# Kernel optimization log

Measured on AMD Instinct MI355X. Metric: run time of the kernel, lower is better.

The kernel has to match this reference:

```python
import jax, jax.numpy as jnp
import numpy as np

N_PAPER, N_AUTHOR, E = 100000, 50000, 1000000
D_PAPER, D_AUTHOR, HID, OUT = 256, 128, 256, 349


def setup_inputs() -> dict:
    key = jax.random.key(0)
    ks = jax.random.split(key, 16)
    s = 0.05
    return {
        'x_paper': jax.random.normal(ks[0], (N_PAPER, D_PAPER), jnp.float32),
        'x_author': jax.random.normal(ks[1], (N_AUTHOR, D_AUTHOR), jnp.float32),
        'cites': jax.random.randint(ks[2], (2, E), 0, N_PAPER, jnp.int64 if jax.config.jax_enable_x64 else jnp.int32),
        'writes_src': jax.random.randint(ks[3], (E,), 0, N_AUTHOR),
        'writes_dst': jax.random.randint(ks[4], (E,), 0, N_PAPER),
        'gcn_W1': jax.random.normal(ks[5], (D_PAPER, HID), jnp.float32) * s,
        'gcn_b1': jnp.zeros((HID,), jnp.float32),
        'sage_Wl1': jax.random.normal(ks[6], (D_AUTHOR, HID), jnp.float32) * s,
        'sage_bl1': jnp.zeros((HID,), jnp.float32),
        'sage_Wr1': jax.random.normal(ks[7], (D_PAPER, HID), jnp.float32) * s,
        'gcn_W2': jax.random.normal(ks[8], (HID, HID), jnp.float32) * s,
        'gcn_b2': jnp.zeros((HID,), jnp.float32),
        'sage_Wl2': jax.random.normal(ks[9], (D_AUTHOR, HID), jnp.float32) * s,
        'sage_bl2': jnp.zeros((HID,), jnp.float32),
        'sage_Wr2': jax.random.normal(ks[10], (HID, HID), jnp.float32) * s,
        'lin_W': jax.random.normal(ks[11], (HID, OUT), jnp.float32) * s,
        'lin_b': jnp.zeros((OUT,), jnp.float32),
    }


def _gcn_conv(x, W, b, src, dst, n):
    # GCNConv with add_self_loops=True, symmetric normalization
    loop = jnp.arange(n, dtype=src.dtype)
    si = jnp.concatenate([src, loop])
    di = jnp.concatenate([dst, loop])
    deg = jax.ops.segment_sum(jnp.ones_like(di, x.dtype), di, n)
    dinv = jnp.where(deg > 0, jax.lax.rsqrt(jnp.maximum(deg, 1.0)), 0.0)
    norm = dinv[si] * dinv[di]  # [E+n]
    h = x @ W                   # [n, hid]
    out = jax.ops.segment_sum(h[si] * norm[:, None], di, n)
    return out + b


def _sage_conv(x_src, x_dst, Wl, bl, Wr, src, dst, n_dst):
    # SAGEConv: mean-aggregate neighbors -> lin_l, plus root lin_r (no bias)
    agg = jax.ops.segment_sum(x_src[src], dst, n_dst)
    cnt = jax.ops.segment_sum(jnp.ones_like(dst, x_src.dtype), dst, n_dst)
    mean = agg / jnp.maximum(cnt, 1.0)[:, None]
    return mean @ Wl + bl + x_dst @ Wr


def reference(x_paper, x_author, cites, writes_src, writes_dst,
              gcn_W1, gcn_b1, sage_Wl1, sage_bl1, sage_Wr1,
              gcn_W2, gcn_b2, sage_Wl2, sage_bl2, sage_Wr2,
              lin_W, lin_b):
    n = x_paper.shape[0]
    c_src, c_dst = cites[0], cites[1]
    # layer 1: HeteroConv with aggr='sum' over the two edge-type outputs
    p = jax.nn.relu(
        _gcn_conv(x_paper, gcn_W1, gcn_b1, c_src, c_dst, n)
        + _sage_conv(x_author, x_paper, sage_Wl1, sage_bl1, sage_Wr1, writes_src, writes_dst, n))
    # layer 2 (author features are never updated by these edge types)
    p = jax.nn.relu(
        _gcn_conv(p, gcn_W2, gcn_b2, c_src, c_dst, n)
        + _sage_conv(x_author, p, sage_Wl2, sage_bl2, sage_Wr2, writes_src, writes_dst, n))
    return p @ lin_W + lin_b
```

## Files before the change

kernel.cpp:

```cpp
#include <hip/hip_runtime.h>


#define DP   256
#define DA   128
#define HIDN 256
#define DOUT 349
#define NBKT 782
#define CHUNK 4096

typedef unsigned short u16;
typedef unsigned int u32;
typedef __attribute__((ext_vector_type(8))) short bf16x8;
typedef __attribute__((ext_vector_type(4))) float f32x4;

__device__ __forceinline__ u16 bf16_rn(float x) {
  union { float f; unsigned u; } v; v.f = x;
  unsigned r = v.u + 0x7FFFu + ((v.u >> 16) & 1u);
  return (u16)(r >> 16);
}
__device__ __forceinline__ float bf16f(u16 h) {
  union { float f; unsigned u; } v; v.u = ((unsigned)h) << 16; return v.f;
}
__device__ __forceinline__ unsigned pack2(float a, float b) {
  return (unsigned)bf16_rn(a) | ((unsigned)bf16_rn(b) << 16);
}

__device__ __forceinline__ void gload16(const void* g, void* lds) {
  __builtin_amdgcn_global_load_lds(
      (const __attribute__((address_space(1))) unsigned int*)g,
      (__attribute__((address_space(3))) unsigned int*)lds, 16, 0, 0);
}

#define SCAN_TPB 256
#define SCAN_VPT 8
#define SCAN_TILE 2048

__global__ void scan_local(const int* __restrict__ in, int* __restrict__ out,
                           int* __restrict__ bsum, int n) {
  __shared__ int sdata[SCAN_TPB];
  int t = threadIdx.x;
  int base = blockIdx.x * SCAN_TILE + t * SCAN_VPT;
  int v[SCAN_VPT];
  int sum = 0;
#pragma unroll
  for (int j = 0; j < SCAN_VPT; ++j) {
    int idx = base + j;
    v[j] = (idx < n) ? in[idx] : 0;
    sum += v[j];
  }
  sdata[t] = sum;
  __syncthreads();
  for (int off = 1; off < SCAN_TPB; off <<= 1) {
    int x = (t >= off) ? sdata[t - off] : 0;
    __syncthreads();
    sdata[t] += x;
    __syncthreads();
  }
  int prefix = sdata[t] - sum;
  if (t == SCAN_TPB - 1) bsum[blockIdx.x] = sdata[t];
  int run = prefix;
#pragma unroll
  for (int j = 0; j < SCAN_VPT; ++j) {
    int idx = base + j;
    if (idx < n) out[idx] = run;
    run += v[j];
  }
}

__global__ void scan_spine(int* __restrict__ bsum, int nb) {
  __shared__ int sdata[256];
  int t = threadIdx.x;
  int v = (t < nb) ? bsum[t] : 0;
  sdata[t] = v;
  __syncthreads();
  for (int off = 1; off < 256; off <<= 1) {
    int x = (t >= off) ? sdata[t - off] : 0;
    __syncthreads();
    sdata[t] += x;
    __syncthreads();
  }
  if (t < nb) bsum[t] = sdata[t] - v;
}

__global__ void scan_add(int* __restrict__ out, const int* __restrict__ bsum, int n) {
  int add = bsum[blockIdx.x];
  int base = blockIdx.x * SCAN_TILE + threadIdx.x * SCAN_VPT;
#pragma unroll
  for (int j = 0; j < SCAN_VPT; ++j) {
    int idx = base + j;
    if (idx < n) out[idx] += add;
  }
}

__global__ __launch_bounds__(256) void sort_pass1(
    const int* __restrict__ c_src, const int* __restrict__ c_dst,
    const int* __restrict__ w_srcP, const int* __restrict__ w_dstP,
    uint2* __restrict__ tmp, int* __restrict__ gcount, int* __restrict__ lofs,
    int E, int nch) {
  const int cg = blockIdx.x, t = threadIdx.x;
  const int et = cg >= nch;
  const int c = cg - et * nch;
  const int* src = et ? w_srcP : c_src;
  const int* dst = et ? w_dstP : c_dst;
  __shared__ u32 cnt[NBKT];
  __shared__ u32 ofs[NBKT];
  __shared__ u32 sdata[256];
  __shared__ uint2 stage[CHUNK];

  for (int i = t; i < NBKT; i += 256) cnt[i] = 0;
  __syncthreads();
  const int base = c * CHUNK;
#pragma unroll
  for (int j = 0; j < 16; ++j) {
    int i = t + j * 256, idx = base + i;
    if (idx < E) {
      uint2 e; e.x = (u32)src[idx]; e.y = (u32)dst[idx];
      stage[i] = e;
      atomicAdd(&cnt[e.y >> 7], 1u);
    }
  }
  __syncthreads();
  for (int i = t; i < NBKT; i += 256)
    gcount[((size_t)et * NBKT + i) * nch + c] = (int)cnt[i];
  u32 ssum = 0;
  const int b0 = t * 4;
#pragma unroll
  for (int j = 0; j < 4; ++j) {
    int i = b0 + j;
    if (i < NBKT) ssum += cnt[i];
  }
  sdata[t] = ssum;
  __syncthreads();
  for (int o = 1; o < 256; o <<= 1) {
    u32 x = (t >= o) ? sdata[t - o] : 0;
    __syncthreads();
    sdata[t] += x;
    __syncthreads();
  }
  u32 run = sdata[t] - ssum;
#pragma unroll
  for (int j = 0; j < 4; ++j) {
    int i = b0 + j;
    if (i < NBKT) { ofs[i] = run; run += cnt[i]; }
  }
  __syncthreads();
  for (int i = t; i < NBKT; i += 256) {
    lofs[((size_t)et * nch + c) * NBKT + i] = (int)ofs[i];
    cnt[i] = ofs[i];
  }
  __syncthreads();
  uint2* tout = tmp + (size_t)et * nch * CHUNK + base;
#pragma unroll
  for (int j = 0; j < 16; ++j) {
    int i = t + j * 256, idx = base + i;
    if (idx < E) {
      uint2 e = stage[i];
      u32 p = atomicAdd(&cnt[e.y >> 7], 1u);
      tout[p] = e;
    }
  }
}

#define MAXB 2560
__global__ __launch_bounds__(256) void sort_pass2(
    const uint2* __restrict__ tmp, const int* __restrict__ prefix,
    const int* __restrict__ gcount, const int* __restrict__ lofs,
    int* __restrict__ cSorted, int* __restrict__ cDeg, int* __restrict__ cOff,
    int* __restrict__ wSorted, int* __restrict__ wDeg, int* __restrict__ wOff,
    float* __restrict__ dinv,
    int E, int nch, int n, int nbk) {
  const int bg = blockIdx.x, t = threadIdx.x;
  const int et = bg >= nbk;
  const int b = bg - et * nbk;
  int* outSorted = et ? wSorted : cSorted;
  int* deg = et ? wDeg : cDeg;
  int* offArr = et ? wOff : cOff;
  __shared__ u32 est[MAXB];
  __shared__ u32 outl[MAXB];
  __shared__ u32 cnt[128], ofs[128];
  __shared__ u32 sdata[256];

  const int node0 = b << 7;
  const size_t bgl = (size_t)et * NBKT + b;
  const int ebaseG = prefix[bgl * nch];
  const int eendG = (bg == 2 * nbk - 1) ? 2 * E : prefix[(bgl + 1) * nch];
  const int ebase = ebaseG - et * E;
  const int esize = (eendG - et * E) - ebase;

  const uint2* tsrc = tmp + (size_t)et * nch * CHUNK;
  for (int c = t; c < nch; c += 256) {
    int g = lofs[((size_t)et * nch + c) * NBKT + b];
    int len = gcount[bgl * nch + c];
    int dp = prefix[bgl * nch + c] - ebaseG;
    for (int k = 0; k < len; ++k) {
      uint2 e = tsrc[(size_t)c * CHUNK + g + k];
      est[dp + k] = (e.x << 7) | (e.y & 127u);
    }
  }
  if (t < 128) cnt[t] = 0;
  __syncthreads();
  for (int i = t; i < esize; i += 256) atomicAdd(&cnt[est[i] & 127u], 1u);
  __syncthreads();
  u32 v = (t < 128) ? cnt[t] : 0;
  sdata[t] = v;
  __syncthreads();
  for (int o = 1; o < 256; o <<= 1) {
    u32 x = (t >= o) ? sdata[t - o] : 0;
    __syncthreads();
    sdata[t] += x;
    __syncthreads();
  }
  if (t < 128) ofs[t] = sdata[t] - v;
  __syncthreads();
  const int nNodes = (n - node0) < 128 ? (n - node0) : 128;
  if (t < nNodes) {
    deg[node0 + t] = (int)cnt[t];
    offArr[node0 + t] = ebase + (int)ofs[t];
    if (et == 0) dinv[node0 + t] = rsqrtf((float)(cnt[t] + 1));
  }
  __syncthreads();
  if (t < 128) cnt[t] = ofs[t];
  __syncthreads();
  for (int i = t; i < esize; i += 256) {
    u32 e = est[i];
    u32 p = atomicAdd(&cnt[e & 127u], 1u);
    outl[p] = e >> 7;
  }
  __syncthreads();
  for (int i = t; i < esize; i += 256) outSorted[ebase + i] = (int)outl[i];
}

__global__ void conv_bf16(const float* __restrict__ x, u16* __restrict__ o, int n8) {
  int i = blockIdx.x * blockDim.x + threadIdx.x;
  if (i >= n8) return;
  const float4* x4 = (const float4*)x;
  float4 v0 = x4[(size_t)i * 2];
  float4 v1 = x4[(size_t)i * 2 + 1];
  uint4 O;
  O.x = pack2(v0.x, v0.y);
  O.y = pack2(v0.z, v0.w);
  O.z = pack2(v1.x, v1.y);
  O.w = pack2(v1.z, v1.w);
  ((uint4*)o)[i] = O;
}

__global__ void prep_weight(const float* __restrict__ W, int K, int N, int Npad,
                            u16* __restrict__ Bt) {
  int idx = blockIdx.x * blockDim.x + threadIdx.x;
  int tot = Npad * K;
  if (idx >= tot) return;
  int n = idx / K, k = idx - n * K;
  float v = (n < N) ? W[(size_t)k * N + n] : 0.f;
  Bt[idx] = bf16_rn(v);
}

__global__ void pad_bias(const float* __restrict__ a, const float* __restrict__ b,
                         float* __restrict__ o, int n, int npad) {
  int i = blockIdx.x * blockDim.x + threadIdx.x;
  if (i < npad) o[i] = (i < n) ? (a[i] + (b ? b[i] : 0.f)) : 0.f;
}

__global__ void gather_fused(
    const u16* __restrict__ xin, const float* __restrict__ dinv,
    const int* __restrict__ c_off, const int* __restrict__ c_cnt,
    const int* __restrict__ c_sorted, u16* __restrict__ xout,
    const u16* __restrict__ xa16, const int* __restrict__ w_off,
    const int* __restrict__ w_cnt, const int* __restrict__ w_sorted,
    u16* __restrict__ mean, int n, int nbw) {
  const int lane = threadIdx.x & 63;
  if (blockIdx.x < nbw) {
    int wave = ((blockIdx.x * blockDim.x) >> 6) + (threadIdx.x >> 6);
    if (wave >= n) return;
    int d = wave;
    int start = c_off[d], cnt = c_cnt[d];
    float a0 = 0.f, a1 = 0.f, a2 = 0.f, a3 = 0.f;
    const uint2* base = (const uint2*)xin;
    for (int j0 = 0; j0 < cnt; j0 += 64) {
      int nn = cnt - j0; nn = nn < 64 ? nn : 64;
      int sl = (j0 + lane < cnt) ? c_sorted[start + j0 + lane] : 0;
      int jj = 0;
      for (; jj + 4 <= nn; jj += 4) {
        int s0 = __shfl(sl, jj), s1 = __shfl(sl, jj + 1);
        int s2 = __shfl(sl, jj + 2), s3 = __shfl(sl, jj + 3);
        float d0 = dinv[s0], d1 = dinv[s1], d2 = dinv[s2], d3 = dinv[s3];
        uint2 v0 = base[(size_t)s0 * 64 + lane];
        uint2 v1 = base[(size_t)s1 * 64 + lane];
        uint2 v2 = base[(size_t)s2 * 64 + lane];
        uint2 v3 = base[(size_t)s3 * 64 + lane];
        a0 = fmaf(bf16f((u16)v0.x), d0, a0); a1 = fmaf(bf16f((u16)(v0.x >> 16)), d0, a1);
        a2 = fmaf(bf16f((u16)v0.y), d0, a2); a3 = fmaf(bf16f((u16)(v0.y >> 16)), d0, a3);
        a0 = fmaf(bf16f((u16)v1.x), d1, a0); a1 = fmaf(bf16f((u16)(v1.x >> 16)), d1, a1);
        a2 = fmaf(bf16f((u16)v1.y), d1, a2); a3 = fmaf(bf16f((u16)(v1.y >> 16)), d1, a3);
        a0 = fmaf(bf16f((u16)v2.x), d2, a0); a1 = fmaf(bf16f((u16)(v2.x >> 16)), d2, a1);
        a2 = fmaf(bf16f((u16)v2.y), d2, a2); a3 = fmaf(bf16f((u16)(v2.y >> 16)), d2, a3);
        a0 = fmaf(bf16f((u16)v3.x), d3, a0); a1 = fmaf(bf16f((u16)(v3.x >> 16)), d3, a1);
        a2 = fmaf(bf16f((u16)v3.y), d3, a2); a3 = fmaf(bf16f((u16)(v3.y >> 16)), d3, a3);
      }
      for (; jj < nn; ++jj) {
        int s = __shfl(sl, jj);
        float ds = dinv[s];
        uint2 v = base[(size_t)s * 64 + lane];
        a0 = fmaf(bf16f((u16)v.x), ds, a0); a1 = fmaf(bf16f((u16)(v.x >> 16)), ds, a1);
        a2 = fmaf(bf16f((u16)v.y), ds, a2); a3 = fmaf(bf16f((u16)(v.y >> 16)), ds, a3);
      }
    }
    float dd = dinv[d];
    {
      uint2 v = base[(size_t)d * 64 + lane];
      a0 = fmaf(bf16f((u16)v.x), dd, a0); a1 = fmaf(bf16f((u16)(v.x >> 16)), dd, a1);
      a2 = fmaf(bf16f((u16)v.y), dd, a2); a3 = fmaf(bf16f((u16)(v.y >> 16)), dd, a3);
    }
    uint2 O;
    O.x = pack2(a0 * dd, a1 * dd);
    O.y = pack2(a2 * dd, a3 * dd);
    ((uint2*)xout)[(size_t)d * 64 + lane] = O;
  } else {
    int wave = (((blockIdx.x - nbw) * blockDim.x) >> 6) + (threadIdx.x >> 6);
    if (wave >= n) return;
    int d = wave;
    int start = w_off[d];
    int cnt = w_cnt[d];
    float ax = 0.f, ay = 0.f;
    const unsigned* xa = (const unsigned*)xa16;
    for (int j0 = 0; j0 < cnt; j0 += 64) {
      int nn = cnt - j0; nn = nn < 64 ? nn : 64;
      int sl = (j0 + lane < cnt) ? w_sorted[start + j0 + lane] : 0;
      int jj = 0;
      for (; jj + 4 <= nn; jj += 4) {
        int s0 = __shfl(sl, jj), s1 = __shfl(sl, jj + 1);
        int s2 = __shfl(sl, jj + 2), s3 = __shfl(sl, jj + 3);
        unsigned v0 = xa[(size_t)s0 * 64 + lane];
        unsigned v1 = xa[(size_t)s1 * 64 + lane];
        unsigned v2 = xa[(size_t)s2 * 64 + lane];
        unsigned v3 = xa[(size_t)s3 * 64 + lane];
        ax += bf16f((u16)v0) + bf16f((u16)v1) + bf16f((u16)v2) + bf16f((u16)v3);
        ay += bf16f((u16)(v0 >> 16)) + bf16f((u16)(v1 >> 16)) +
              bf16f((u16)(v2 >> 16)) + bf16f((u16)(v3 >> 16));
      }
      for (; jj < nn; ++jj) {
        int s = __shfl(sl, jj);
        unsigned v = xa[(size_t)s * 64 + lane];
        ax += bf16f((u16)v);
        ay += bf16f((u16)(v >> 16));
      }
    }
    float inv = 1.0f / (float)((cnt > 0) ? cnt : 1);
    ((unsigned*)mean)[(size_t)d * 64 + lane] = pack2(ax * inv, ay * inv);
  }
}

__global__ void agg_gcn(const u16* __restrict__ xin, const float* __restrict__ dinv,
                        const int* __restrict__ c_off, const int* __restrict__ c_cnt,
                        const int* __restrict__ c_sorted,
                        u16* __restrict__ xout, int n) {
  int wave = (blockIdx.x * blockDim.x + threadIdx.x) >> 6;
  int lane = threadIdx.x & 63;
  if (wave >= n) return;
  int d = wave;
  int start = c_off[d], cnt = c_cnt[d];
  float a0 = 0.f, a1 = 0.f, a2 = 0.f, a3 = 0.f;
  const uint2* base = (const uint2*)xin;
  for (int j0 = 0; j0 < cnt; j0 += 64) {
    int nn = cnt - j0; nn = nn < 64 ? nn : 64;
    int sl = (j0 + lane < cnt) ? c_sorted[start + j0 + lane] : 0;
    int jj = 0;
    for (; jj + 4 <= nn; jj += 4) {
      int s0 = __shfl(sl, jj), s1 = __shfl(sl, jj + 1);
      int s2 = __shfl(sl, jj + 2), s3 = __shfl(sl, jj + 3);
      float d0 = dinv[s0], d1 = dinv[s1], d2 = dinv[s2], d3 = dinv[s3];
      uint2 v0 = base[(size_t)s0 * 64 + lane];
      uint2 v1 = base[(size_t)s1 * 64 + lane];
      uint2 v2 = base[(size_t)s2 * 64 + lane];
      uint2 v3 = base[(size_t)s3 * 64 + lane];
      a0 = fmaf(bf16f((u16)v0.x), d0, a0); a1 = fmaf(bf16f((u16)(v0.x >> 16)), d0, a1);
      a2 = fmaf(bf16f((u16)v0.y), d0, a2); a3 = fmaf(bf16f((u16)(v0.y >> 16)), d0, a3);
      a0 = fmaf(bf16f((u16)v1.x), d1, a0); a1 = fmaf(bf16f((u16)(v1.x >> 16)), d1, a1);
      a2 = fmaf(bf16f((u16)v1.y), d1, a2); a3 = fmaf(bf16f((u16)(v1.y >> 16)), d1, a3);
      a0 = fmaf(bf16f((u16)v2.x), d2, a0); a1 = fmaf(bf16f((u16)(v2.x >> 16)), d2, a1);
      a2 = fmaf(bf16f((u16)v2.y), d2, a2); a3 = fmaf(bf16f((u16)(v2.y >> 16)), d2, a3);
      a0 = fmaf(bf16f((u16)v3.x), d3, a0); a1 = fmaf(bf16f((u16)(v3.x >> 16)), d3, a1);
      a2 = fmaf(bf16f((u16)v3.y), d3, a2); a3 = fmaf(bf16f((u16)(v3.y >> 16)), d3, a3);
    }
    for (; jj < nn; ++jj) {
      int s = __shfl(sl, jj);
      float ds = dinv[s];
      uint2 v = base[(size_t)s * 64 + lane];
      a0 = fmaf(bf16f((u16)v.x), ds, a0); a1 = fmaf(bf16f((u16)(v.x >> 16)), ds, a1);
      a2 = fmaf(bf16f((u16)v.y), ds, a2); a3 = fmaf(bf16f((u16)(v.y >> 16)), ds, a3);
    }
  }
  float dd = dinv[d];
  {
    uint2 v = base[(size_t)d * 64 + lane];
    a0 = fmaf(bf16f((u16)v.x), dd, a0); a1 = fmaf(bf16f((u16)(v.x >> 16)), dd, a1);
    a2 = fmaf(bf16f((u16)v.y), dd, a2); a3 = fmaf(bf16f((u16)(v.y >> 16)), dd, a3);
  }
  uint2 O;
  O.x = pack2(a0 * dd, a1 * dd);
  O.y = pack2(a2 * dd, a3 * dd);
  ((uint2*)xout)[(size_t)d * 64 + lane] = O;
}

template <int NSEG, bool F32OUT, int NC>
__global__ __launch_bounds__(256, 4) void gemm_bf16(
    const u16* __restrict__ A0, const u16* __restrict__ A1, const u16* __restrict__ A2,
    const u16* __restrict__ B0, const u16* __restrict__ B1, const u16* __restrict__ B2,
    const float* __restrict__ bias,
    u16* __restrict__ Cp, float* __restrict__ Cf,
    int M, int N) {
  __shared__ u16 Ah[2][4096];
  __shared__ u16 Bh[2][4096];

  const int t = threadIdx.x;
  const int wid = t >> 6, lane = t & 63;
  const int wr = wid >> 1, wc = wid & 1;
  const int lrow = lane & 15, kslot = lane >> 4;
  const int jsw = kslot ^ ((lrow >> 1) & 3);

  const int nb = gridDim.x;
  const int q = nb >> 3, r = nb & 7;
  const int xcd = blockIdx.x & 7, pos = blockIdx.x >> 3;
  const int lin = (xcd < r ? xcd * (q + 1) : r * (q + 1) + (xcd - r) * q) + pos;
  const int bx = lin / NC, by = lin - bx * NC;
  const int gm = bx * 128;
  const int gn = by * 128;

  const int s_r = lane >> 2;
  const int s_j = (lane & 3) ^ ((s_r >> 1) & 3);

  f32x4 acc[4][4];
  const f32x4 z4 = {0.f, 0.f, 0.f, 0.f};
#pragma unroll
  for (int m = 0; m < 4; ++m)
#pragma unroll
    for (int n = 0; n < 4; ++n) acc[m][n] = z4;

  const int NT = (NSEG == 3) ? 20 : 8;

  auto STAGE = [&](int tt, int half) {
    const u16* A;
    const u16* B;
    int rs, k0;
    if (NSEG == 3 && tt >= 16)     { A = A2; B = B2; rs = 128; k0 = (tt - 16) * 32; }
    else if (NSEG == 3 && tt >= 8) { A = A1; B = B1; rs = 256; k0 = (tt - 8) * 32; }
    else                           { A = A0; B = B0; rs = 256; k0 = tt * 32; }
    const int c = wid * 2;
#pragma unroll
    for (int cc = 0; cc < 2; ++cc) {
      int grow = gm + (c + cc) * 16 + s_r;
      grow = grow < M ? grow : M - 1;
      gload16(A + (size_t)grow * rs + (k0 + s_j * 8), &Ah[half][(c + cc) * 512]);
      int col = gn + (c + cc) * 16 + s_r;
      gload16(B + (size_t)col * rs + (k0 + s_j * 8), &Bh[half][(c + cc) * 512]);
    }
  };

  STAGE(0, 0);
  __syncthreads();

  for (int tt = 0; tt < NT; ++tt) {
    const int half = tt & 1;
    if (tt + 1 < NT) STAGE(tt + 1, half ^ 1);

    bf16x8 ah[4];
    const int ab = (wr * 64 + lrow) * 32 + jsw * 8;
#pragma unroll
    for (int m = 0; m < 4; ++m) ah[m] = *(const bf16x8*)&Ah[half][ab + m * 512];
    const int bb = (wc * 64 + lrow) * 32 + jsw * 8;
#pragma unroll
    for (int n = 0; n < 4; ++n) {
      bf16x8 bn = *(const bf16x8*)&Bh[half][bb + n * 512];
#pragma unroll
      for (int m = 0; m < 4; ++m)
        acc[m][n] = __builtin_amdgcn_mfma_f32_16x16x32_bf16(ah[m], bn, acc[m][n], 0, 0, 0);
    }
    __syncthreads();
  }

  const int col0 = gn + wc * 64 + lrow;
  const int row00 = gm + wr * 64 + kslot * 4;
#pragma unroll
  for (int m = 0; m < 4; ++m) {
#pragma unroll
    for (int i = 0; i < 4; ++i) {
      int row = row00 + m * 16 + i;
      if (row >= M) continue;
#pragma unroll
      for (int n = 0; n < 4; ++n) {
        int col = col0 + n * 16;
        float v = acc[m][n][i] + bias[col];
        if (F32OUT) {
          if (col < N) Cf[(size_t)row * N + col] = v;
        } else {
          Cp[(size_t)row * 256 + col] = bf16_rn(fmaxf(v, 0.f));
        }
      }
    }
  }
}

static inline size_t align_up(size_t x) { return (x + 255) & ~(size_t)255; }

extern "C" void kernel_launch(void* const* d_in, const int* in_sizes, int n_in,
                              void* d_out, int out_size, void* d_ws, size_t ws_size,
                              hipStream_t stream) {
  const float* x_paper  = (const float*)d_in[0];
  const float* x_author = (const float*)d_in[1];
  const int*   cites    = (const int*)d_in[2];
  const int*   w_src    = (const int*)d_in[3];
  const int*   w_dst    = (const int*)d_in[4];
  const float* W1  = (const float*)d_in[5];
  const float* b1  = (const float*)d_in[6];
  const float* Wl1 = (const float*)d_in[7];
  const float* bl1 = (const float*)d_in[8];
  const float* Wr1 = (const float*)d_in[9];
  const float* W2  = (const float*)d_in[10];
  const float* b2  = (const float*)d_in[11];
  const float* Wl2 = (const float*)d_in[12];
  const float* bl2 = (const float*)d_in[13];
  const float* Wr2 = (const float*)d_in[14];
  const float* linW = (const float*)d_in[15];
  const float* linb = (const float*)d_in[16];
  float* out = (float*)d_out;

  const int N = in_sizes[0] / DP;
  const int NA = in_sizes[1] / DA;
  const int E = in_sizes[3];
  const int* c_src = cites;
  const int* c_dst = cites + E;

  const int NCH = (E + CHUNK - 1) / CHUNK;
  const int NB = (N + 127) >> 7;
  const int GC2 = 2 * NB * NCH;

  char* w = (char*)d_ws;
  size_t off = 0;
  auto alloc = [&](size_t bytes) -> void* {
    void* p = w + off;
    off = align_up(off + bytes);
    return p;
  };
  int* deg_c      = (int*)alloc((size_t)N * 4);
  int* cnt_w      = (int*)alloc((size_t)N * 4);
  int* cites_off  = (int*)alloc((size_t)N * 4);
  int* writes_off = (int*)alloc((size_t)N * 4);
  int* c_sorted   = (int*)alloc((size_t)E * 4);
  int* w_sorted   = (int*)alloc((size_t)E * 4);
  uint2* tmpE     = (uint2*)alloc((size_t)2 * NCH * CHUNK * 8);
  int* gcount     = (int*)alloc((size_t)GC2 * 4);
  int* gprefix    = (int*)alloc((size_t)GC2 * 4);
  int* lofs       = (int*)alloc((size_t)2 * NCH * NBKT * 4);
  int* bsumA      = (int*)alloc(256 * 4);
  float* dinv     = (float*)alloc((size_t)N * 4);
  u16* xa16       = (u16*)alloc((size_t)NA * DA * 2);
  u16* meanA      = (u16*)alloc((size_t)N * DA * 2);
  u16* xp         = (u16*)alloc((size_t)N * 256 * 2);
  u16* xs         = (u16*)alloc((size_t)N * 256 * 2);
  u16* pb         = (u16*)alloc((size_t)N * 256 * 2);
  const int bsW = 256 * 256, bsL = 256 * 128, bsLin = 384 * 256;
  u16* BtW1  = (u16*)alloc((size_t)bsW * 2);
  u16* BtWr1 = (u16*)alloc((size_t)bsW * 2);
  u16* BtW2  = (u16*)alloc((size_t)bsW * 2);
  u16* BtWr2 = (u16*)alloc((size_t)bsW * 2);
  u16* BtWl1 = (u16*)alloc((size_t)bsL * 2);
  u16* BtWl2 = (u16*)alloc((size_t)bsL * 2);
  u16* BtLin = (u16*)alloc((size_t)bsLin * 2);
  float* biasR1  = (float*)alloc(256 * 4);
  float* biasR2  = (float*)alloc(256 * 4);
  float* biasLin = (float*)alloc(384 * 4);
  (void)ws_size; (void)n_in; (void)out_size;

  const int nsb2 = (GC2 + SCAN_TILE - 1) / SCAN_TILE;

  sort_pass1<<<2 * NCH, 256, 0, stream>>>(c_src, c_dst, w_src, w_dst,
                                          tmpE, gcount, lofs, E, NCH);
  scan_local<<<nsb2, SCAN_TPB, 0, stream>>>(gcount, gprefix, bsumA, GC2);
  scan_spine<<<1, 256, 0, stream>>>(bsumA, nsb2);
  scan_add<<<nsb2, SCAN_TPB, 0, stream>>>(gprefix, bsumA, GC2);
  sort_pass2<<<2 * NB, 256, 0, stream>>>(tmpE, gprefix, gcount, lofs,
                                         c_sorted, deg_c, cites_off,
                                         w_sorted, cnt_w, writes_off,
                                         dinv, E, NCH, N, NB);

  conv_bf16<<<(N * 32 + 255) / 256, 256, 0, stream>>>(x_paper, xp, N * 32);
  conv_bf16<<<(NA * 16 + 255) / 256, 256, 0, stream>>>(x_author, xa16, NA * 16);

  prep_weight<<<(bsW + 255) / 256, 256, 0, stream>>>(W1, 256, 256, 256, BtW1);
  prep_weight<<<(bsW + 255) / 256, 256, 0, stream>>>(Wr1, 256, 256, 256, BtWr1);
  prep_weight<<<(bsW + 255) / 256, 256, 0, stream>>>(W2, 256, 256, 256, BtW2);
  prep_weight<<<(bsW + 255) / 256, 256, 0, stream>>>(Wr2, 256, 256, 256, BtWr2);
  prep_weight<<<(bsL + 255) / 256, 256, 0, stream>>>(Wl1, 128, 256, 256, BtWl1);
  prep_weight<<<(bsL + 255) / 256, 256, 0, stream>>>(Wl2, 128, 256, 256, BtWl2);
  prep_weight<<<(bsLin + 255) / 256, 256, 0, stream>>>(linW, 256, DOUT, 384, BtLin);
  pad_bias<<<1, 256, 0, stream>>>(b1, bl1, biasR1, 256, 256);
  pad_bias<<<1, 256, 0, stream>>>(b2, bl2, biasR2, 256, 256);
  pad_bias<<<2, 256, 0, stream>>>(linb, nullptr, biasLin, DOUT, 384);

  const int nbWave = (N * 64 + 255) / 256;
  const int GX = (N + 127) / 128;

  gather_fused<<<2 * nbWave, 256, 0, stream>>>(
      xp, dinv, cites_off, deg_c, c_sorted, xs,
      xa16, writes_off, cnt_w, w_sorted, meanA, N, nbWave);
  gemm_bf16<3, false, 2><<<GX * 2, 256, 0, stream>>>(
      xs, xp, meanA, BtW1, BtWr1, BtWl1, biasR1, pb, nullptr, N, HIDN);
  agg_gcn<<<nbWave, 256, 0, stream>>>(pb, dinv, cites_off, deg_c, c_sorted, xs, N);
  gemm_bf16<3, false, 2><<<GX * 2, 256, 0, stream>>>(
      xs, pb, meanA, BtW2, BtWr2, BtWl2, biasR2, xp, nullptr, N, HIDN);
  gemm_bf16<1, true, 3><<<GX * 3, 256, 0, stream>>>(
      xp, nullptr, nullptr, BtLin, nullptr, nullptr, biasLin, nullptr, out, N, DOUT);
}
```

Measured before the change: 493.2 us.

## Pack sort payload into 32 bits, merge prep launches, deepen gather unroll

The sort passes now carry one packed 32-bit payload (src<<7 | dst&127) per edge plus a 16-bit bucket index in shared memory, which halves the temp-buffer traffic between sort_pass1 and sort_pass2. The ten separate conversion, weight-prep and bias kernels are merged into a single prep_all launch to cut launch overhead. The GCN and mean gather loops are moved into shared helpers and unrolled by 8 instead of 4 for more memory-level parallelism, at the cost of higher register pressure. The packed payload assumes source indices fit in 25 bits.

```diff
diff --git a/kernel.cpp b/kernel.cpp
--- a/kernel.cpp
+++ b/kernel.cpp
@@ -95,7 +95,7 @@
 __global__ __launch_bounds__(256) void sort_pass1(
     const int* __restrict__ c_src, const int* __restrict__ c_dst,
     const int* __restrict__ w_srcP, const int* __restrict__ w_dstP,
-    uint2* __restrict__ tmp, int* __restrict__ gcount, int* __restrict__ lofs,
+    u32* __restrict__ tmp, int* __restrict__ gcount, int* __restrict__ lofs,
     int E, int nch) {
   const int cg = blockIdx.x, t = threadIdx.x;
   const int et = cg >= nch;
@@ -105,7 +105,8 @@
   __shared__ u32 cnt[NBKT];
   __shared__ u32 ofs[NBKT];
   __shared__ u32 sdata[256];
-  __shared__ uint2 stage[CHUNK];
+  __shared__ u32 pay[CHUNK];
+  __shared__ u16 bkt[CHUNK];
 
   for (int i = t; i < NBKT; i += 256) cnt[i] = 0;
   __syncthreads();
@@ -114,9 +115,10 @@
   for (int j = 0; j < 16; ++j) {
     int i = t + j * 256, idx = base + i;
     if (idx < E) {
-      uint2 e; e.x = (u32)src[idx]; e.y = (u32)dst[idx];
-      stage[i] = e;
-      atomicAdd(&cnt[e.y >> 7], 1u);
+      u32 s = (u32)src[idx], d = (u32)dst[idx];
+      pay[i] = (s << 7) | (d & 127u);
+      bkt[i] = (u16)(d >> 7);
+      atomicAdd(&cnt[d >> 7], 1u);
     }
   }
   __syncthreads();
@@ -149,21 +151,20 @@
     cnt[i] = ofs[i];
   }
   __syncthreads();
-  uint2* tout = tmp + (size_t)et * nch * CHUNK + base;
+  u32* tout = tmp + (size_t)et * nch * CHUNK + base;
 #pragma unroll
   for (int j = 0; j < 16; ++j) {
     int i = t + j * 256, idx = base + i;
     if (idx < E) {
-      uint2 e = stage[i];
-      u32 p = atomicAdd(&cnt[e.y >> 7], 1u);
-      tout[p] = e;
+      u32 p = atomicAdd(&cnt[bkt[i]], 1u);
+      tout[p] = pay[i];
     }
   }
 }
 
 #define MAXB 2560
 __global__ __launch_bounds__(256) void sort_pass2(
-    const uint2* __restrict__ tmp, const int* __restrict__ prefix,
+    const u32* __restrict__ tmp, const int* __restrict__ prefix,
     const int* __restrict__ gcount, const int* __restrict__ lofs,
     int* __restrict__ cSorted, int* __restrict__ cDeg, int* __restrict__ cOff,
     int* __restrict__ wSorted, int* __restrict__ wDeg, int* __restrict__ wOff,
@@ -187,15 +188,13 @@
   const int ebase = ebaseG - et * E;
   const int esize = (eendG - et * E) - ebase;
 
-  const uint2* tsrc = tmp + (size_t)et * nch * CHUNK;
+  const u32* tsrc = tmp + (size_t)et * nch * CHUNK;
   for (int c = t; c < nch; c += 256) {
     int g = lofs[((size_t)et * nch + c) * NBKT + b];
     int len = gcount[bgl * nch + c];
     int dp = prefix[bgl * nch + c] - ebaseG;
-    for (int k = 0; k < len; ++k) {
-      uint2 e = tsrc[(size_t)c * CHUNK + g + k];
-      est[dp + k] = (e.x << 7) | (e.y & 127u);
-    }
+    for (int k = 0; k < len; ++k)
+      est[dp + k] = tsrc[(size_t)c * CHUNK + g + k];
   }
   if (t < 128) cnt[t] = 0;
   __syncthreads();
@@ -230,34 +229,159 @@
   for (int i = t; i < esize; i += 256) outSorted[ebase + i] = (int)outl[i];
 }
 
-__global__ void conv_bf16(const float* __restrict__ x, u16* __restrict__ o, int n8) {
-  int i = blockIdx.x * blockDim.x + threadIdx.x;
-  if (i >= n8) return;
-  const float4* x4 = (const float4*)x;
-  float4 v0 = x4[(size_t)i * 2];
-  float4 v1 = x4[(size_t)i * 2 + 1];
-  uint4 O;
-  O.x = pack2(v0.x, v0.y);
-  O.y = pack2(v0.z, v0.w);
-  O.z = pack2(v1.x, v1.y);
-  O.w = pack2(v1.z, v1.w);
-  ((uint4*)o)[i] = O;
-}
-
-__global__ void prep_weight(const float* __restrict__ W, int K, int N, int Npad,
-                            u16* __restrict__ Bt) {
-  int idx = blockIdx.x * blockDim.x + threadIdx.x;
+__global__ void prep_all(
+    const float* __restrict__ x_paper, const float* __restrict__ x_author,
+    u16* __restrict__ xp, u16* __restrict__ xa16,
+    const float* __restrict__ W1, const float* __restrict__ Wr1,
+    const float* __restrict__ W2, const float* __restrict__ Wr2,
+    const float* __restrict__ Wl1, const float* __restrict__ Wl2,
+    const float* __restrict__ linW,
+    u16* __restrict__ BtW1, u16* __restrict__ BtWr1,
+    u16* __restrict__ BtW2, u16* __restrict__ BtWr2,
+    u16* __restrict__ BtWl1, u16* __restrict__ BtWl2, u16* __restrict__ BtLin,
+    const float* __restrict__ b1, const float* __restrict__ bl1,
+    const float* __restrict__ b2, const float* __restrict__ bl2,
+    const float* __restrict__ linb,
+    float* __restrict__ biasR1, float* __restrict__ biasR2,
+    float* __restrict__ biasLin,
+    int N, int NA) {
+  const int R1 = (N * 32 + 255) / 256;
+  const int R2 = R1 + (NA * 16 + 255) / 256;
+  const int WB = 256 * 256 / 256;
+  const int LB = 256 * 128 / 256;
+  const int FB = 384 * 256 / 256;
+  int bid = blockIdx.x, t = threadIdx.x;
+
+  if (bid < R1) {
+    int i = bid * 256 + t;
+    if (i < N * 32) {
+      const float4* x4 = (const float4*)x_paper;
+      float4 v0 = x4[(size_t)i * 2];
+      float4 v1 = x4[(size_t)i * 2 + 1];
+      uint4 O;
+      O.x = pack2(v0.x, v0.y); O.y = pack2(v0.z, v0.w);
+      O.z = pack2(v1.x, v1.y); O.w = pack2(v1.z, v1.w);
+      ((uint4*)xp)[i] = O;
+    }
+    return;
+  }
+  if (bid < R2) {
+    int i = (bid - R1) * 256 + t;
+    if (i < NA * 16) {
+      const float4* x4 = (const float4*)x_author;
+      float4 v0 = x4[(size_t)i * 2];
+      float4 v1 = x4[(size_t)i * 2 + 1];
+      uint4 O;
+      O.x = pack2(v0.x, v0.y); O.y = pack2(v0.z, v0.w);
+      O.z = pack2(v1.x, v1.y); O.w = pack2(v1.z, v1.w);
+      ((uint4*)xa16)[i] = O;
+    }
+    return;
+  }
+  int wb = bid - R2;
+  const float* W; u16* Bt; int K, Nn, Npad;
+  if      (wb < WB)                  { W = W1;  Bt = BtW1;  K = 256; Nn = 256; Npad = 256; }
+  else if ((wb -= WB) < WB)          { W = Wr1; Bt = BtWr1; K = 256; Nn = 256; Npad = 256; }
+  else if ((wb -= WB) < WB)          { W = W2;  Bt = BtW2;  K = 256; Nn = 256; Npad = 256; }
+  else if ((wb -= WB) < WB)          { W = Wr2; Bt = BtWr2; K = 256; Nn = 256; Npad = 256; }
+  else if ((wb -= WB) < LB)          { W = Wl1; Bt = BtWl1; K = 128; Nn = 256; Npad = 256; }
+  else if ((wb -= LB) < LB)          { W = Wl2; Bt = BtWl2; K = 128; Nn = 256; Npad = 256; }
+  else if ((wb -= LB) < FB)          { W = linW; Bt = BtLin; K = 256; Nn = DOUT; Npad = 384; }
+  else {
+    if (t < 256) {
+      biasR1[t] = b1[t] + bl1[t];
+      biasR2[t] = b2[t] + bl2[t];
+    }
+    for (int i = t; i < 384; i += 256) biasLin[i] = (i < DOUT) ? linb[i] : 0.f;
+    return;
+  }
+  int idx = wb * 256 + t;
   int tot = Npad * K;
   if (idx >= tot) return;
-  int n = idx / K, k = idx - n * K;
-  float v = (n < N) ? W[(size_t)k * N + n] : 0.f;
+  int nn = idx / K, k = idx - nn * K;
+  float v = (nn < Nn) ? W[(size_t)k * Nn + nn] : 0.f;
   Bt[idx] = bf16_rn(v);
 }
 
-__global__ void pad_bias(const float* __restrict__ a, const float* __restrict__ b,
-                         float* __restrict__ o, int n, int npad) {
-  int i = blockIdx.x * blockDim.x + threadIdx.x;
-  if (i < npad) o[i] = (i < n) ? (a[i] + (b ? b[i] : 0.f)) : 0.f;
+__device__ __forceinline__ void agg_body(
+    const uint2* __restrict__ base, const float* __restrict__ dinv,
+    const int* __restrict__ c_off, const int* __restrict__ c_cnt,
+    const int* __restrict__ c_sorted, u16* __restrict__ xout,
+    int d, int lane) {
+  int start = c_off[d], cnt = c_cnt[d];
+  float a0 = 0.f, a1 = 0.f, a2 = 0.f, a3 = 0.f;
+  for (int j0 = 0; j0 < cnt; j0 += 64) {
+    int nn = cnt - j0; nn = nn < 64 ? nn : 64;
+    int sl = (j0 + lane < cnt) ? c_sorted[start + j0 + lane] : 0;
+    int jj = 0;
+    for (; jj + 8 <= nn; jj += 8) {
+      int ss[8]; float dv[8]; uint2 vv[8];
+#pragma unroll
+      for (int u = 0; u < 8; ++u) ss[u] = __shfl(sl, jj + u);
+#pragma unroll
+      for (int u = 0; u < 8; ++u) dv[u] = dinv[ss[u]];
+#pragma unroll
+      for (int u = 0; u < 8; ++u) vv[u] = base[(size_t)ss[u] * 64 + lane];
+#pragma unroll
+      for (int u = 0; u < 8; ++u) {
+        a0 = fmaf(bf16f((u16)vv[u].x), dv[u], a0);
+        a1 = fmaf(bf16f((u16)(vv[u].x >> 16)), dv[u], a1);
+        a2 = fmaf(bf16f((u16)vv[u].y), dv[u], a2);
+        a3 = fmaf(bf16f((u16)(vv[u].y >> 16)), dv[u], a3);
+      }
+    }
+    for (; jj < nn; ++jj) {
+      int s = __shfl(sl, jj);
+      float ds = dinv[s];
+      uint2 v = base[(size_t)s * 64 + lane];
+      a0 = fmaf(bf16f((u16)v.x), ds, a0); a1 = fmaf(bf16f((u16)(v.x >> 16)), ds, a1);
+      a2 = fmaf(bf16f((u16)v.y), ds, a2); a3 = fmaf(bf16f((u16)(v.y >> 16)), ds, a3);
+    }
+  }
+  float dd = dinv[d];
+  {
+    uint2 v = base[(size_t)d * 64 + lane];
+    a0 = fmaf(bf16f((u16)v.x), dd, a0); a1 = fmaf(bf16f((u16)(v.x >> 16)), dd, a1);
+    a2 = fmaf(bf16f((u16)v.y), dd, a2); a3 = fmaf(bf16f((u16)(v.y >> 16)), dd, a3);
+  }
+  uint2 O;
+  O.x = pack2(a0 * dd, a1 * dd);
+  O.y = pack2(a2 * dd, a3 * dd);
+  ((uint2*)xout)[(size_t)d * 64 + lane] = O;
+}
+
+__device__ __forceinline__ void mean_body(
+    const unsigned* __restrict__ xa, const int* __restrict__ w_off,
+    const int* __restrict__ w_cnt, const int* __restrict__ w_sorted,
+    u16* __restrict__ mean, int d, int lane) {
+  int start = w_off[d];
+  int cnt = w_cnt[d];
+  float ax = 0.f, ay = 0.f;
+  for (int j0 = 0; j0 < cnt; j0 += 64) {
+    int nn = cnt - j0; nn = nn < 64 ? nn : 64;
+    int sl = (j0 + lane < cnt) ? w_sorted[start + j0 + lane] : 0;
+    int jj = 0;
+    for (; jj + 8 <= nn; jj += 8) {
+      int ss[8]; unsigned vv[8];
+#pragma unroll
+      for (int u = 0; u < 8; ++u) ss[u] = __shfl(sl, jj + u);
+#pragma unroll
+      for (int u = 0; u < 8; ++u) vv[u] = xa[(size_t)ss[u] * 64 + lane];
+#pragma unroll
+      for (int u = 0; u < 8; ++u) {
+        ax += bf16f((u16)vv[u]);
+        ay += bf16f((u16)(vv[u] >> 16));
+      }
+    }
+    for (; jj < nn; ++jj) {
+      int s = __shfl(sl, jj);
+      unsigned v = xa[(size_t)s * 64 + lane];
+      ax += bf16f((u16)v);
+      ay += bf16f((u16)(v >> 16));
+    }
+  }
+  float inv = 1.0f / (float)((cnt > 0) ? cnt : 1);
+  ((unsigned*)mean)[(size_t)d * 64 + lane] = pack2(ax * inv, ay * inv);
 }
 
 __global__ void gather_fused(
@@ -269,83 +393,13 @@
     u16* __restrict__ mean, int n, int nbw) {
   const int lane = threadIdx.x & 63;
   if (blockIdx.x < nbw) {
-    int wave = ((blockIdx.x * blockDim.x) >> 6) + (threadIdx.x >> 6);
-    if (wave >= n) return;
-    int d = wave;
-    int start = c_off[d], cnt = c_cnt[d];
-    float a0 = 0.f, a1 = 0.f, a2 = 0.f, a3 = 0.f;
-    const uint2* base = (const uint2*)xin;
-    for (int j0 = 0; j0 < cnt; j0 += 64) {
-      int nn = cnt - j0; nn = nn < 64 ? nn : 64;
-      int sl = (j0 + lane < cnt) ? c_sorted[start + j0 + lane] : 0;
-      int jj = 0;
-      for (; jj + 4 <= nn; jj += 4) {
-        int s0 = __shfl(sl, jj), s1 = __shfl(sl, jj + 1);
-        int s2 = __shfl(sl, jj + 2), s3 = __shfl(sl, jj + 3);
-        float d0 = dinv[s0], d1 = dinv[s1], d2 = dinv[s2], d3 = dinv[s3];
-        uint2 v0 = base[(size_t)s0 * 64 + lane];
-        uint2 v1 = base[(size_t)s1 * 64 + lane];
-        uint2 v2 = base[(size_t)s2 * 64 + lane];
-        uint2 v3 = base[(size_t)s3 * 64 + lane];
-        a0 = fmaf(bf16f((u16)v0.x), d0, a0); a1 = fmaf(bf16f((u16)(v0.x >> 16)), d0, a1);
-        a2 = fmaf(bf16f((u16)v0.y), d0, a2); a3 = fmaf(bf16f((u16)(v0.y >> 16)), d0, a3);
-        a0 = fmaf(bf16f((u16)v1.x), d1, a0); a1 = fmaf(bf16f((u16)(v1.x >> 16)), d1, a1);
-        a2 = fmaf(bf16f((u16)v1.y), d1, a2); a3 = fmaf(bf16f((u16)(v1.y >> 16)), d1, a3);
-        a0 = fmaf(bf16f((u16)v2.x), d2, a0); a1 = fmaf(bf16f((u16)(v2.x >> 16)), d2, a1);
-        a2 = fmaf(bf16f((u16)v2.y), d2, a2); a3 = fmaf(bf16f((u16)(v2.y >> 16)), d2, a3);
-        a0 = fmaf(bf16f((u16)v3.x), d3, a0); a1 = fmaf(bf16f((u16)(v3.x >> 16)), d3, a1);
-        a2 = fmaf(bf16f((u16)v3.y), d3, a2); a3 = fmaf(bf16f((u16)(v3.y >> 16)), d3, a3);
-      }
-      for (; jj < nn; ++jj) {
-        int s = __shfl(sl, jj);
-        float ds = dinv[s];
-        uint2 v = base[(size_t)s * 64 + lane];
-        a0 = fmaf(bf16f((u16)v.x), ds, a0); a1 = fmaf(bf16f((u16)(v.x >> 16)), ds, a1);
-        a2 = fmaf(bf16f((u16)v.y), ds, a2); a3 = fmaf(bf16f((u16)(v.y >> 16)), ds, a3);
-      }
-    }
-    float dd = dinv[d];
-    {
-      uint2 v = base[(size_t)d * 64 + lane];
-      a0 = fmaf(bf16f((u16)v.x), dd, a0); a1 = fmaf(bf16f((u16)(v.x >> 16)), dd, a1);
-      a2 = fmaf(bf16f((u16)v.y), dd, a2); a3 = fmaf(bf16f((u16)(v.y >> 16)), dd, a3);
-    }
-    uint2 O;
-    O.x = pack2(a0 * dd, a1 * dd);
-    O.y = pack2(a2 * dd, a3 * dd);
-    ((uint2*)xout)[(size_t)d * 64 + lane] = O;
+    int d = ((blockIdx.x * blockDim.x) >> 6) + (threadIdx.x >> 6);
+    if (d >= n) return;
+    agg_body((const uint2*)xin, dinv, c_off, c_cnt, c_sorted, xout, d, lane);
   } else {
-    int wave = (((blockIdx.x - nbw) * blockDim.x) >> 6) + (threadIdx.x >> 6);
-    if (wave >= n) return;
-    int d = wave;
-    int start = w_off[d];
-    int cnt = w_cnt[d];
-    float ax = 0.f, ay = 0.f;
-    const unsigned* xa = (const unsigned*)xa16;
-    for (int j0 = 0; j0 < cnt; j0 += 64) {
-      int nn = cnt - j0; nn = nn < 64 ? nn : 64;
-      int sl = (j0 + lane < cnt) ? w_sorted[start + j0 + lane] : 0;
-      int jj = 0;
-      for (; jj + 4 <= nn; jj += 4) {
-        int s0 = __shfl(sl, jj), s1 = __shfl(sl, jj + 1);
-        int s2 = __shfl(sl, jj + 2), s3 = __shfl(sl, jj + 3);
-        unsigned v0 = xa[(size_t)s0 * 64 + lane];
-        unsigned v1 = xa[(size_t)s1 * 64 + lane];
-        unsigned v2 = xa[(size_t)s2 * 64 + lane];
-        unsigned v3 = xa[(size_t)s3 * 64 + lane];
-        ax += bf16f((u16)v0) + bf16f((u16)v1) + bf16f((u16)v2) + bf16f((u16)v3);
-        ay += bf16f((u16)(v0 >> 16)) + bf16f((u16)(v1 >> 16)) +
-              bf16f((u16)(v2 >> 16)) + bf16f((u16)(v3 >> 16));
-      }
-      for (; jj < nn; ++jj) {
-        int s = __shfl(sl, jj);
-        unsigned v = xa[(size_t)s * 64 + lane];
-        ax += bf16f((u16)v);
-        ay += bf16f((u16)(v >> 16));
-      }
-    }
-    float inv = 1.0f / (float)((cnt > 0) ? cnt : 1);
-    ((unsigned*)mean)[(size_t)d * 64 + lane] = pack2(ax * inv, ay * inv);
+    int d = (((blockIdx.x - nbw) * blockDim.x) >> 6) + (threadIdx.x >> 6);
+    if (d >= n) return;
+    mean_body((const unsigned*)xa16, w_off, w_cnt, w_sorted, mean, d, lane);
   }
 }
 
@@ -353,52 +407,10 @@
                         const int* __restrict__ c_off, const int* __restrict__ c_cnt,
                         const int* __restrict__ c_sorted,
                         u16* __restrict__ xout, int n) {
-  int wave = (blockIdx.x * blockDim.x + threadIdx.x) >> 6;
+  int d = (blockIdx.x * blockDim.x + threadIdx.x) >> 6;
   int lane = threadIdx.x & 63;
-  if (wave >= n) return;
-  int d = wave;
-  int start = c_off[d], cnt = c_cnt[d];
-  float a0 = 0.f, a1 = 0.f, a2 = 0.f, a3 = 0.f;
-  const uint2* base = (const uint2*)xin;
-  for (int j0 = 0; j0 < cnt; j0 += 64) {
-    int nn = cnt - j0; nn = nn < 64 ? nn : 64;
-    int sl = (j0 + lane < cnt) ? c_sorted[start + j0 + lane] : 0;
-    int jj = 0;
-    for (; jj + 4 <= nn; jj += 4) {
-      int s0 = __shfl(sl, jj), s1 = __shfl(sl, jj + 1);
-      int s2 = __shfl(sl, jj + 2), s3 = __shfl(sl, jj + 3);
-      float d0 = dinv[s0], d1 = dinv[s1], d2 = dinv[s2], d3 = dinv[s3];
-      uint2 v0 = base[(size_t)s0 * 64 + lane];
-      uint2 v1 = base[(size_t)s1 * 64 + lane];
-      uint2 v2 = base[(size_t)s2 * 64 + lane];
-      uint2 v3 = base[(size_t)s3 * 64 + lane];
-      a0 = fmaf(bf16f((u16)v0.x), d0, a0); a1 = fmaf(bf16f((u16)(v0.x >> 16)), d0, a1);
-      a2 = fmaf(bf16f((u16)v0.y), d0, a2); a3 = fmaf(bf16f((u16)(v0.y >> 16)), d0, a3);
-      a0 = fmaf(bf16f((u16)v1.x), d1, a0); a1 = fmaf(bf16f((u16)(v1.x >> 16)), d1, a1);
-      a2 = fmaf(bf16f((u16)v1.y), d1, a2); a3 = fmaf(bf16f((u16)(v1.y >> 16)), d1, a3);
-      a0 = fmaf(bf16f((u16)v2.x), d2, a0); a1 = fmaf(bf16f((u16)(v2.x >> 16)), d2, a1);
-      a2 = fmaf(bf16f((u16)v2.y), d2, a2); a3 = fmaf(bf16f((u16)(v2.y >> 16)), d2, a3);
-      a0 = fmaf(bf16f((u16)v3.x), d3, a0); a1 = fmaf(bf16f((u16)(v3.x >> 16)), d3, a1);
-      a2 = fmaf(bf16f((u16)v3.y), d3, a2); a3 = fmaf(bf16f((u16)(v3.y >> 16)), d3, a3);
-    }
-    for (; jj < nn; ++jj) {
-      int s = __shfl(sl, jj);
-      float ds = dinv[s];
-      uint2 v = base[(size_t)s * 64 + lane];
-      a0 = fmaf(bf16f((u16)v.x), ds, a0); a1 = fmaf(bf16f((u16)(v.x >> 16)), ds, a1);
-      a2 = fmaf(bf16f((u16)v.y), ds, a2); a3 = fmaf(bf16f((u16)(v.y >> 16)), ds, a3);
-    }
-  }
-  float dd = dinv[d];
-  {
-    uint2 v = base[(size_t)d * 64 + lane];
-    a0 = fmaf(bf16f((u16)v.x), dd, a0); a1 = fmaf(bf16f((u16)(v.x >> 16)), dd, a1);
-    a2 = fmaf(bf16f((u16)v.y), dd, a2); a3 = fmaf(bf16f((u16)(v.y >> 16)), dd, a3);
-  }
-  uint2 O;
-  O.x = pack2(a0 * dd, a1 * dd);
-  O.y = pack2(a2 * dd, a3 * dd);
-  ((uint2*)xout)[(size_t)d * 64 + lane] = O;
+  if (d >= n) return;
+  agg_body((const uint2*)xin, dinv, c_off, c_cnt, c_sorted, xout, d, lane);
 }
 
 template <int NSEG, bool F32OUT, int NC>
@@ -546,7 +558,7 @@
   int* writes_off = (int*)alloc((size_t)N * 4);
   int* c_sorted   = (int*)alloc((size_t)E * 4);
   int* w_sorted   = (int*)alloc((size_t)E * 4);
-  uint2* tmpE     = (uint2*)alloc((size_t)2 * NCH * CHUNK * 8);
+  u32* tmpE       = (u32*)alloc((size_t)2 * NCH * CHUNK * 4);
   int* gcount     = (int*)alloc((size_t)GC2 * 4);
   int* gprefix    = (int*)alloc((size_t)GC2 * 4);
   int* lofs       = (int*)alloc((size_t)2 * NCH * NBKT * 4);
@@ -582,19 +594,16 @@
                                          w_sorted, cnt_w, writes_off,
                                          dinv, E, NCH, N, NB);
 
-  conv_bf16<<<(N * 32 + 255) / 256, 256, 0, stream>>>(x_paper, xp, N * 32);
-  conv_bf16<<<(NA * 16 + 255) / 256, 256, 0, stream>>>(x_author, xa16, NA * 16);
-
-  prep_weight<<<(bsW + 255) / 256, 256, 0, stream>>>(W1, 256, 256, 256, BtW1);
-  prep_weight<<<(bsW + 255) / 256, 256, 0, stream>>>(Wr1, 256, 256, 256, BtWr1);
-  prep_weight<<<(bsW + 255) / 256, 256, 0, stream>>>(W2, 256, 256, 256, BtW2);
-  prep_weight<<<(bsW + 255) / 256, 256, 0, stream>>>(Wr2, 256, 256, 256, BtWr2);
-  prep_weight<<<(bsL + 255) / 256, 256, 0, stream>>>(Wl1, 128, 256, 256, BtWl1);
-  prep_weight<<<(bsL + 255) / 256, 256, 0, stream>>>(Wl2, 128, 256, 256, BtWl2);
-  prep_weight<<<(bsLin + 255) / 256, 256, 0, stream>>>(linW, 256, DOUT, 384, BtLin);
-  pad_bias<<<1, 256, 0, stream>>>(b1, bl1, biasR1, 256, 256);
-  pad_bias<<<1, 256, 0, stream>>>(b2, bl2, biasR2, 256, 256);
-  pad_bias<<<2, 256, 0, stream>>>(linb, nullptr, biasLin, DOUT, 384);
+  {
+    const int R1 = (N * 32 + 255) / 256;
+    const int R2 = R1 + (NA * 16 + 255) / 256;
+    const int total = R2 + 4 * 256 + 2 * 128 + 384 + 1;
+    prep_all<<<total, 256, 0, stream>>>(
+        x_paper, x_author, xp, xa16,
+        W1, Wr1, W2, Wr2, Wl1, Wl2, linW,
+        BtW1, BtWr1, BtW2, BtWr2, BtWl1, BtWl2, BtLin,
+        b1, bl1, b2, bl2, linb, biasR1, biasR2, biasLin, N, NA);
+  }
 
   const int nbWave = (N * 64 + 255) / 256;
   const int GX = (N + 127) / 128;
```

Result: faster. 471.3 us (-4.4%).
